# Optimization experiments

Hardware: AMD Instinct MI355X
Metric: run time of the kernel (lower is better)

The kernel has to match this reference:

```python
import jax, jax.numpy as jnp
import numpy as np

N_POS = 8192
BATCH = 4
N_GT = 512
EPS = 1e-6
P_EXP = -1.0  # generalized-mean exponent (p < 0)


def setup_inputs() -> dict:
    key = jax.random.key(0)
    k1, k2, k3 = jax.random.split(key, 3)
    dis_matrix = jax.random.uniform(k1, (N_POS, N_POS), dtype=jnp.float32)
    prob_map = jax.random.uniform(k2, (BATCH, N_POS), dtype=jnp.float32)
    gt = jax.random.randint(k3, (BATCH, N_GT), 0, N_POS, dtype=jnp.int64 if jax.config.jax_enable_x64 else jnp.int32)
    return {"prob_map": prob_map, "gt": gt, "dis_matrix": dis_matrix}


def reference(prob_map, gt, dis_matrix):
    max_dist = jnp.max(dis_matrix)
    # global min-max normalization with detached min/range (matches torch .detach())
    pmin = jax.lax.stop_gradient(jnp.min(prob_map))
    prange = jax.lax.stop_gradient(jnp.max(prob_map) - jnp.min(prob_map))
    prob = jnp.clip((prob_map - pmin) / prange, 0.0, 1.0)  # (B, N)

    # gather gt-indexed columns: dis_matrix[:, gt] -> (N, B, G) -> (B, N, G)
    D = jnp.transpose(jnp.take(dis_matrix, gt, axis=1), (1, 0, 2))

    n_est = prob.sum(axis=1)  # (B,)
    # term 1: (1/n_est) * sum_n p_n * min_g D[n, g]
    term1 = jnp.sum(prob * jnp.min(D, axis=2), axis=1) / (n_est + EPS)  # (B,)

    # term 2: generalized mean over pixel dim of weighted distance matrix
    w = (1.0 - prob)[:, :, None] * max_dist + prob[:, :, None] * D  # (B, N, G)
    minn = jnp.mean((w + EPS) ** P_EXP, axis=1) ** (1.0 / P_EXP)  # (B, G)
    term2 = jnp.mean(minn, axis=1)  # (B,)

    return jnp.mean(term1) + jnp.mean(term2)
```

## Files before the change

kernel.cpp:

```cpp
#include <hip/hip_runtime.h>
#include <math.h>

#define N_POS 8192
#define BATCH 4
#define N_GT 512
#define BG (BATCH * N_GT)
#define EPSV 1e-6f

#define WS_PART_MAX 0
#define WS_SC 2048
#define WS_S 2064
#define WS_T1 4112
#define K1_BLOCKS 2048

__global__ __launch_bounds__(256) void whd_k1_max(const float4* __restrict__ dis,
                                                  float* __restrict__ part) {
    int t = threadIdx.x;
    long gid = (long)blockIdx.x * blockDim.x + t;
    long stride = (long)gridDim.x * blockDim.x;
    long n4 = ((long)N_POS * N_POS) / 4;
    float m = -INFINITY;
    for (long i = gid; i < n4; i += stride) {
        float4 v = dis[i];
        m = fmaxf(m, fmaxf(fmaxf(v.x, v.y), fmaxf(v.z, v.w)));
    }
    #pragma unroll
    for (int off = 32; off; off >>= 1) m = fmaxf(m, __shfl_down(m, off, 64));
    __shared__ float sm[4];
    if ((t & 63) == 0) sm[t >> 6] = m;
    __syncthreads();
    if (t == 0) {
        float mm = fmaxf(fmaxf(sm[0], sm[1]), fmaxf(sm[2], sm[3]));
        part[blockIdx.x] = mm;
    }
}

__global__ __launch_bounds__(1024) void whd_k2_scalars(const float* __restrict__ prob,
                                                       float* __restrict__ wsf) {
    __shared__ float red[1024];
    int t = threadIdx.x;
    float m = -INFINITY;
    for (int i = t; i < K1_BLOCKS; i += 1024) m = fmaxf(m, wsf[WS_PART_MAX + i]);
    red[t] = m; __syncthreads();
    for (int s = 512; s; s >>= 1) { if (t < s) red[t] = fmaxf(red[t], red[t + s]); __syncthreads(); }
    float maxdist = red[0]; __syncthreads();
    float lmin = INFINITY, lmax = -INFINITY;
    for (int i = t; i < BATCH * N_POS; i += 1024) {
        float v = prob[i];
        lmin = fminf(lmin, v); lmax = fmaxf(lmax, v);
    }
    red[t] = lmin; __syncthreads();
    for (int s = 512; s; s >>= 1) { if (t < s) red[t] = fminf(red[t], red[t + s]); __syncthreads(); }
    float pmin = red[0]; __syncthreads();
    red[t] = lmax; __syncthreads();
    for (int s = 512; s; s >>= 1) { if (t < s) red[t] = fmaxf(red[t], red[t + s]); __syncthreads(); }
    float pmax = red[0]; __syncthreads();
    float prange = pmax - pmin;
    float inv = 1.0f / prange;
    for (int b = 0; b < BATCH; b++) {
        float s = 0.f;
        for (int i = t; i < N_POS; i += 1024) {
            float p = (prob[b * N_POS + i] - pmin) * inv;
            p = fminf(fmaxf(p, 0.f), 1.f);
            s += p;
        }
        red[t] = s; __syncthreads();
        for (int st = 512; st; st >>= 1) { if (t < st) red[t] += red[t + st]; __syncthreads(); }
        if (t == 0) wsf[WS_SC + 3 + b] = red[0];
        __syncthreads();
    }
    if (t == 0) {
        wsf[WS_SC + 0] = maxdist;
        wsf[WS_SC + 1] = pmin;
        wsf[WS_SC + 2] = prange;
    }
    for (int i = t; i < BG; i += 1024) wsf[WS_S + i] = 0.f;
    if (t < BATCH) wsf[WS_T1 + t] = 0.f;
}

#define ROWS_PER_BLOCK 16
__global__ __launch_bounds__(256) void whd_k3_main(const float* __restrict__ dis,
                                                   const float* __restrict__ prob,
                                                   const int* __restrict__ gt,
                                                   float* __restrict__ wsf) {
    __shared__ float rowbuf[N_POS];
    __shared__ int gtl[BG];
    __shared__ float minsh[4][4];
    int t = threadIdx.x;
    int wv = t >> 6, lane = t & 63;
    int row0 = blockIdx.x * ROWS_PER_BLOCK;
    for (int i = t; i < BG; i += 256) gtl[i] = gt[i];
    float maxd = wsf[WS_SC + 0];
    float pmin = wsf[WS_SC + 1];
    float invr = 1.0f / wsf[WS_SC + 2];
    __syncthreads();
    int c[8];
    #pragma unroll
    for (int k = 0; k < 8; k++) c[k] = gtl[t + 256 * k];
    float acc[8];
    #pragma unroll
    for (int k = 0; k < 8; k++) acc[k] = 0.f;
    float t1sum = 0.f;

    for (int r = 0; r < ROWS_PER_BLOCK; r++) {
        int n = row0 + r;
        __syncthreads();
        const float4* src = (const float4*)(dis + (size_t)n * N_POS);
        float4* dstl = (float4*)rowbuf;
        for (int i = t; i < N_POS / 4; i += 256) dstl[i] = src[i];
        float pb[4];
        #pragma unroll
        for (int b = 0; b < BATCH; b++) {
            float p = (prob[b * N_POS + n] - pmin) * invr;
            pb[b] = fminf(fmaxf(p, 0.f), 1.f);
        }
        __syncthreads();
        float vmin[4];
        #pragma unroll
        for (int k = 0; k < 8; k++) {
            float v = rowbuf[c[k]];
            int b = k >> 1;
            float w = fmaf(pb[b], v - maxd, maxd) + EPSV;
            acc[k] += 1.0f / w;
            if ((k & 1) == 0) vmin[b] = v; else vmin[b] = fminf(vmin[b], v);
        }
        #pragma unroll
        for (int b = 0; b < BATCH; b++) {
            float m = vmin[b];
            #pragma unroll
            for (int off = 32; off; off >>= 1) m = fminf(m, __shfl_xor(m, off, 64));
            if (lane == 0) minsh[wv][b] = m;
        }
        __syncthreads();
        if (t < BATCH) {
            float m = fminf(fminf(minsh[0][t], minsh[1][t]), fminf(minsh[2][t], minsh[3][t]));
            t1sum += pb[t] * m;
        }
    }
    #pragma unroll
    for (int k = 0; k < 8; k++) atomicAdd(&wsf[WS_S + t + 256 * k], acc[k]);
    if (t < BATCH) atomicAdd(&wsf[WS_T1 + t], t1sum);
}

__global__ __launch_bounds__(256) void whd_k4_out(const float* __restrict__ wsf,
                                                  float* __restrict__ out) {
    __shared__ float red[256];
    int t = threadIdx.x;
    float s = 0.f;
    for (int i = t; i < BG; i += 256) s += (float)N_POS / wsf[WS_S + i];
    red[t] = s; __syncthreads();
    for (int st = 128; st; st >>= 1) { if (t < st) red[t] += red[t + st]; __syncthreads(); }
    if (t == 0) {
        float term2 = red[0] / (float)BG;
        float term1 = 0.f;
        for (int b = 0; b < BATCH; b++)
            term1 += wsf[WS_T1 + b] / (wsf[WS_SC + 3 + b] + EPSV);
        term1 *= (1.0f / BATCH);
        out[0] = term1 + term2;
    }
}

extern "C" void kernel_launch(void* const* d_in, const int* in_sizes, int n_in,
                              void* d_out, int out_size, void* d_ws, size_t ws_size,
                              hipStream_t stream) {
    const float* prob = (const float*)d_in[0];
    const int* gt = (const int*)d_in[1];
    const float* dis = (const float*)d_in[2];
    float* out = (float*)d_out;
    float* wsf = (float*)d_ws;

    whd_k1_max<<<K1_BLOCKS, 256, 0, stream>>>((const float4*)dis, wsf + WS_PART_MAX);
    whd_k2_scalars<<<1, 1024, 0, stream>>>(prob, wsf);
    whd_k3_main<<<N_POS / ROWS_PER_BLOCK, 256, 0, stream>>>(dis, prob, gt, wsf);
    whd_k4_out<<<1, 256, 0, stream>>>(wsf, out);
}
```

Baseline: 453.5 us.

## Fuse global max with gt-column gather in one pass over distance matrix

The old code read the 256MB distance matrix twice: once to find its global max and again to gather the gt columns. The new version reads it once, computing partial maxes while writing a packed (N, B*G) gather and per-row min distances to workspace. Later kernels compute term1 from the stored mins and the generalized mean from the 64MB packed buffer. Per-column atomics are replaced with partial-sum buffers and a separate column reduction. This removes one full matrix read but adds a 64MB write and reread plus extra kernel launches.

```diff
diff --git a/kernel.cpp b/kernel.cpp
--- a/kernel.cpp
+++ b/kernel.cpp
@@ -7,40 +7,91 @@
 #define BG (BATCH * N_GT)
 #define EPSV 1e-6f
 
-#define WS_PART_MAX 0
-#define WS_SC 2048
-#define WS_S 2064
-#define WS_T1 4112
-#define K1_BLOCKS 2048
-
-__global__ __launch_bounds__(256) void whd_k1_max(const float4* __restrict__ dis,
-                                                  float* __restrict__ part) {
-    int t = threadIdx.x;
-    long gid = (long)blockIdx.x * blockDim.x + t;
-    long stride = (long)gridDim.x * blockDim.x;
-    long n4 = ((long)N_POS * N_POS) / 4;
+#define WS_DPACK 0
+#define WS_PARTS 16777216
+#define WS_MIND  18874368
+#define WS_PMAX  18907136
+#define WS_SC    18908160
+
+#define KA_BLOCKS 1024
+#define ROWS_A 8
+#define KC_BLOCKS 1024
+#define ROWS_C 8
+
+__global__ __launch_bounds__(256) void whd_kA(const float* __restrict__ dis,
+                                              const int* __restrict__ gt,
+                                              float* __restrict__ wsf) {
+    __shared__ float rowbuf[N_POS];
+    __shared__ unsigned short gtl[BG];
+    __shared__ float minsh[4][4];
+    __shared__ float smax[4];
+    int t = threadIdx.x;
+    int wv = t >> 6, lane = t & 63;
+    int row0 = blockIdx.x * ROWS_A;
+    float* dpack = wsf + WS_DPACK;
+    float* minD = wsf + WS_MIND;
+
+    for (int i = t; i < BG; i += 256) gtl[i] = (unsigned short)gt[i];
+    __syncthreads();
+    int c[8];
+    #pragma unroll
+    for (int k = 0; k < 8; k++) c[k] = gtl[t + 256 * k];
+
+    float tmax = -INFINITY;
+    for (int r = 0; r < ROWS_A; r++) {
+        int n = row0 + r;
+        if (r > 0) {
+            __syncthreads();
+            if (t < BATCH) {
+                float m = fminf(fminf(minsh[0][t], minsh[1][t]), fminf(minsh[2][t], minsh[3][t]));
+                minD[t * N_POS + (n - 1)] = m;
+            }
+        }
+        const float4* src = (const float4*)(dis + (size_t)n * N_POS);
+        float4* dstl = (float4*)rowbuf;
+        #pragma unroll
+        for (int j = 0; j < N_POS / 4 / 256; j++) {
+            int i = t + 256 * j;
+            float4 v = src[i];
+            tmax = fmaxf(tmax, fmaxf(fmaxf(v.x, v.y), fmaxf(v.z, v.w)));
+            dstl[i] = v;
+        }
+        __syncthreads();
+        float vmin[4];
+        #pragma unroll
+        for (int k = 0; k < 8; k++) {
+            float v = rowbuf[c[k]];
+            dpack[(size_t)n * BG + t + 256 * k] = v;
+            int b = k >> 1;
+            if ((k & 1) == 0) vmin[b] = v; else vmin[b] = fminf(vmin[b], v);
+        }
+        #pragma unroll
+        for (int b = 0; b < BATCH; b++) {
+            float m = vmin[b];
+            #pragma unroll
+            for (int off = 32; off; off >>= 1) m = fminf(m, __shfl_xor(m, off, 64));
+            if (lane == 0) minsh[wv][b] = m;
+        }
+    }
+    __syncthreads();
+    if (t < BATCH) {
+        float m = fminf(fminf(minsh[0][t], minsh[1][t]), fminf(minsh[2][t], minsh[3][t]));
+        minD[t * N_POS + (row0 + ROWS_A - 1)] = m;
+    }
+    #pragma unroll
+    for (int off = 32; off; off >>= 1) tmax = fmaxf(tmax, __shfl_down(tmax, off, 64));
+    if (lane == 0) smax[wv] = tmax;
+    __syncthreads();
+    if (t == 0)
+        wsf[WS_PMAX + blockIdx.x] = fmaxf(fmaxf(smax[0], smax[1]), fmaxf(smax[2], smax[3]));
+}
+
+__global__ __launch_bounds__(1024) void whd_kB1(const float* __restrict__ prob,
+                                                float* __restrict__ wsf) {
+    __shared__ float red[1024];
+    int t = threadIdx.x;
     float m = -INFINITY;
-    for (long i = gid; i < n4; i += stride) {
-        float4 v = dis[i];
-        m = fmaxf(m, fmaxf(fmaxf(v.x, v.y), fmaxf(v.z, v.w)));
-    }
-    #pragma unroll
-    for (int off = 32; off; off >>= 1) m = fmaxf(m, __shfl_down(m, off, 64));
-    __shared__ float sm[4];
-    if ((t & 63) == 0) sm[t >> 6] = m;
-    __syncthreads();
-    if (t == 0) {
-        float mm = fmaxf(fmaxf(sm[0], sm[1]), fmaxf(sm[2], sm[3]));
-        part[blockIdx.x] = mm;
-    }
-}
-
-__global__ __launch_bounds__(1024) void whd_k2_scalars(const float* __restrict__ prob,
-                                                       float* __restrict__ wsf) {
-    __shared__ float red[1024];
-    int t = threadIdx.x;
-    float m = -INFINITY;
-    for (int i = t; i < K1_BLOCKS; i += 1024) m = fmaxf(m, wsf[WS_PART_MAX + i]);
+    for (int i = t; i < KA_BLOCKS; i += 1024) m = fmaxf(m, wsf[WS_PMAX + i]);
     red[t] = m; __syncthreads();
     for (int s = 512; s; s >>= 1) { if (t < s) red[t] = fmaxf(red[t], red[t + s]); __syncthreads(); }
     float maxdist = red[0]; __syncthreads();
@@ -54,108 +105,96 @@
     float pmin = red[0]; __syncthreads();
     red[t] = lmax; __syncthreads();
     for (int s = 512; s; s >>= 1) { if (t < s) red[t] = fmaxf(red[t], red[t + s]); __syncthreads(); }
-    float pmax = red[0]; __syncthreads();
-    float prange = pmax - pmin;
-    float inv = 1.0f / prange;
-    for (int b = 0; b < BATCH; b++) {
-        float s = 0.f;
-        for (int i = t; i < N_POS; i += 1024) {
-            float p = (prob[b * N_POS + i] - pmin) * inv;
-            p = fminf(fmaxf(p, 0.f), 1.f);
-            s += p;
-        }
-        red[t] = s; __syncthreads();
-        for (int st = 512; st; st >>= 1) { if (t < st) red[t] += red[t + st]; __syncthreads(); }
-        if (t == 0) wsf[WS_SC + 3 + b] = red[0];
-        __syncthreads();
-    }
+    float pmax = red[0];
     if (t == 0) {
         wsf[WS_SC + 0] = maxdist;
         wsf[WS_SC + 1] = pmin;
-        wsf[WS_SC + 2] = prange;
-    }
-    for (int i = t; i < BG; i += 1024) wsf[WS_S + i] = 0.f;
-    if (t < BATCH) wsf[WS_T1 + t] = 0.f;
-}
-
-#define ROWS_PER_BLOCK 16
-__global__ __launch_bounds__(256) void whd_k3_main(const float* __restrict__ dis,
-                                                   const float* __restrict__ prob,
-                                                   const int* __restrict__ gt,
-                                                   float* __restrict__ wsf) {
-    __shared__ float rowbuf[N_POS];
-    __shared__ int gtl[BG];
-    __shared__ float minsh[4][4];
-    int t = threadIdx.x;
-    int wv = t >> 6, lane = t & 63;
-    int row0 = blockIdx.x * ROWS_PER_BLOCK;
-    for (int i = t; i < BG; i += 256) gtl[i] = gt[i];
+        wsf[WS_SC + 2] = pmax - pmin;
+    }
+    if (t >= 3 && t < 12) wsf[WS_SC + t] = 0.f;
+}
+
+__global__ __launch_bounds__(128) void whd_kB2(const float* __restrict__ prob,
+                                               float* __restrict__ wsf) {
+    __shared__ float sred[2];
+    int t = threadIdx.x;
+    int n = blockIdx.x * 128 + t;
+    float pmin = wsf[WS_SC + 1];
+    float invr = 1.0f / wsf[WS_SC + 2];
+    const float* minD = wsf + WS_MIND;
+    #pragma unroll
+    for (int b = 0; b < BATCH; b++) {
+        float p = (prob[b * N_POS + n] - pmin) * invr;
+        p = fminf(fmaxf(p, 0.f), 1.f);
+        float pm = p * minD[b * N_POS + n];
+        #pragma unroll
+        for (int off = 32; off; off >>= 1) {
+            p += __shfl_down(p, off, 64);
+            pm += __shfl_down(pm, off, 64);
+        }
+        if ((t & 63) == 0) { if (t == 64) { sred[0] = p; sred[1] = pm; } }
+        __syncthreads();
+        if (t == 0) {
+            atomicAdd(&wsf[WS_SC + 3 + b], p + sred[0]);
+            atomicAdd(&wsf[WS_SC + 7 + b], pm + sred[1]);
+        }
+        __syncthreads();
+    }
+}
+
+__global__ __launch_bounds__(256) void whd_kC(const float* __restrict__ prob,
+                                              float* __restrict__ wsf) {
+    int t = threadIdx.x;
+    int row0 = blockIdx.x * ROWS_C;
+    const float* dpack = wsf + WS_DPACK;
     float maxd = wsf[WS_SC + 0];
     float pmin = wsf[WS_SC + 1];
     float invr = 1.0f / wsf[WS_SC + 2];
-    __syncthreads();
-    int c[8];
-    #pragma unroll
-    for (int k = 0; k < 8; k++) c[k] = gtl[t + 256 * k];
     float acc[8];
     #pragma unroll
     for (int k = 0; k < 8; k++) acc[k] = 0.f;
-    float t1sum = 0.f;
-
-    for (int r = 0; r < ROWS_PER_BLOCK; r++) {
+    for (int r = 0; r < ROWS_C; r++) {
         int n = row0 + r;
-        __syncthreads();
-        const float4* src = (const float4*)(dis + (size_t)n * N_POS);
-        float4* dstl = (float4*)rowbuf;
-        for (int i = t; i < N_POS / 4; i += 256) dstl[i] = src[i];
         float pb[4];
         #pragma unroll
         for (int b = 0; b < BATCH; b++) {
             float p = (prob[b * N_POS + n] - pmin) * invr;
             pb[b] = fminf(fmaxf(p, 0.f), 1.f);
         }
-        __syncthreads();
-        float vmin[4];
+        const float* rowp = dpack + (size_t)n * BG;
         #pragma unroll
         for (int k = 0; k < 8; k++) {
-            float v = rowbuf[c[k]];
-            int b = k >> 1;
-            float w = fmaf(pb[b], v - maxd, maxd) + EPSV;
+            float d = rowp[t + 256 * k];
+            float w = fmaf(pb[k >> 1], d - maxd, maxd) + EPSV;
             acc[k] += 1.0f / w;
-            if ((k & 1) == 0) vmin[b] = v; else vmin[b] = fminf(vmin[b], v);
-        }
-        #pragma unroll
-        for (int b = 0; b < BATCH; b++) {
-            float m = vmin[b];
-            #pragma unroll
-            for (int off = 32; off; off >>= 1) m = fminf(m, __shfl_xor(m, off, 64));
-            if (lane == 0) minsh[wv][b] = m;
-        }
-        __syncthreads();
-        if (t < BATCH) {
-            float m = fminf(fminf(minsh[0][t], minsh[1][t]), fminf(minsh[2][t], minsh[3][t]));
-            t1sum += pb[t] * m;
-        }
-    }
-    #pragma unroll
-    for (int k = 0; k < 8; k++) atomicAdd(&wsf[WS_S + t + 256 * k], acc[k]);
-    if (t < BATCH) atomicAdd(&wsf[WS_T1 + t], t1sum);
-}
-
-__global__ __launch_bounds__(256) void whd_k4_out(const float* __restrict__ wsf,
-                                                  float* __restrict__ out) {
+        }
+    }
+    float* outp = wsf + WS_PARTS + (size_t)blockIdx.x * BG;
+    #pragma unroll
+    for (int k = 0; k < 8; k++) outp[t + 256 * k] = acc[k];
+}
+
+__global__ __launch_bounds__(256) void whd_kD(float* __restrict__ wsf) {
     __shared__ float red[256];
     int t = threadIdx.x;
+    int col = blockIdx.x * 256 + t;
+    const float* parts = wsf + WS_PARTS;
     float s = 0.f;
-    for (int i = t; i < BG; i += 256) s += (float)N_POS / wsf[WS_S + i];
-    red[t] = s; __syncthreads();
+    for (int ch = 0; ch < KC_BLOCKS; ch++) s += parts[(size_t)ch * BG + col];
+    float val = (float)N_POS / s;
+    red[t] = val; __syncthreads();
     for (int st = 128; st; st >>= 1) { if (t < st) red[t] += red[t + st]; __syncthreads(); }
-    if (t == 0) {
-        float term2 = red[0] / (float)BG;
+    if (t == 0) atomicAdd(&wsf[WS_SC + 11], red[0]);
+}
+
+__global__ __launch_bounds__(64) void whd_kE(const float* __restrict__ wsf,
+                                             float* __restrict__ out) {
+    if (threadIdx.x == 0) {
         float term1 = 0.f;
         for (int b = 0; b < BATCH; b++)
-            term1 += wsf[WS_T1 + b] / (wsf[WS_SC + 3 + b] + EPSV);
+            term1 += wsf[WS_SC + 7 + b] / (wsf[WS_SC + 3 + b] + EPSV);
         term1 *= (1.0f / BATCH);
+        float term2 = wsf[WS_SC + 11] * (1.0f / BG);
         out[0] = term1 + term2;
     }
 }
@@ -169,8 +208,10 @@
     float* out = (float*)d_out;
     float* wsf = (float*)d_ws;
 
-    whd_k1_max<<<K1_BLOCKS, 256, 0, stream>>>((const float4*)dis, wsf + WS_PART_MAX);
-    whd_k2_scalars<<<1, 1024, 0, stream>>>(prob, wsf);
-    whd_k3_main<<<N_POS / ROWS_PER_BLOCK, 256, 0, stream>>>(dis, prob, gt, wsf);
-    whd_k4_out<<<1, 256, 0, stream>>>(wsf, out);
-}
+    whd_kA<<<KA_BLOCKS, 256, 0, stream>>>(dis, gt, wsf);
+    whd_kB1<<<1, 1024, 0, stream>>>(prob, wsf);
+    whd_kB2<<<N_POS / 128, 128, 0, stream>>>(prob, wsf);
+    whd_kC<<<KC_BLOCKS, 256, 0, stream>>>(prob, wsf);
+    whd_kD<<<BG / 256, 256, 0, stream>>>(wsf);
+    whd_kE<<<1, 64, 0, stream>>>(wsf, out);
+}
```

Result: slower. 472.5 us (+4.2%).
